# Kernel optimization log

Measured on AMD Instinct MI355X. Metric: run time of the kernel, lower is better.

The kernel has to match this reference:

```python
import jax, jax.numpy as jnp
import numpy as np

T, H, I = 8192, 4096, 11008  # tokens, hidden, intermediate (LLaMA-7B)


def setup_inputs() -> dict:
    key = jax.random.key(0)
    ks = jax.random.split(key, 8)
    # int8-valued tensors stored as int32 (spec dtype enum lacks int8)
    hidden_states = jax.random.randint(ks[0], (T, H), -128, 128, dtype=jnp.int32)
    gate_w = jax.random.randint(ks[1], (I, H), -128, 128, dtype=jnp.int32)
    up_w = jax.random.randint(ks[2], (I, H), -128, 128, dtype=jnp.int32)
    down_w = jax.random.randint(ks[3], (H, I), -128, 128, dtype=jnp.int32)
    # per-tensor dequant scales (alpha = input_scale * weight_scale); small so
    # the SwiGLU product lands roughly in int8 range before requantization
    gate_a = jnp.float32(0.004)
    up_a = jnp.float32(0.004)
    down_a = jnp.float32(0.004)
    gate_b = jax.random.normal(ks[4], (I,), dtype=jnp.float32)
    up_b = jax.random.normal(ks[5], (I,), dtype=jnp.float32)
    down_b = jax.random.normal(ks[6], (H,), dtype=jnp.float32)
    return dict(hidden_states=hidden_states, gate_w=gate_w, gate_a=gate_a,
                gate_b=gate_b, up_w=up_w, up_a=up_a, up_b=up_b,
                down_w=down_w, down_a=down_a, down_b=down_b)


def _w8a8_linear(x_i8, w_i8, alpha, bias):
    # scale alpha and fp32 bias (W8A8BFP32OFP32Linear semantics).
    acc = jnp.matmul(x_i8.astype(jnp.int8), w_i8.astype(jnp.int8).T,
                     preferred_element_type=jnp.int32)
    return acc.astype(jnp.float32) * alpha + bias


def reference(hidden_states, gate_w, gate_a, gate_b, up_w, up_a, up_b,
              down_w, down_a, down_b):
    x1 = jax.nn.silu(_w8a8_linear(hidden_states, gate_w, gate_a, gate_b))  # [T,I]
    x2 = _w8a8_linear(hidden_states, up_w, up_a, up_b)                     # [T,I]
    x = x1 * x2
    # requantize: round, clamp to int8 range
    q = jnp.clip(jnp.round(x), -128.0, 127.0).astype(jnp.int32)
    return _w8a8_linear(q, down_w, down_a, down_b)                          # [T,H]
```

## Files before the change

kernel.cpp:

```cpp
#include <hip/hip_runtime.h>
#include <math.h>

#define T_DIM 8192
#define H_DIM 4096
#define I_DIM 11008

typedef int v4i  __attribute__((ext_vector_type(4)));
typedef int v16i __attribute__((ext_vector_type(16)));

#define AS1(p) ((const __attribute__((address_space(1))) void*)(p))
#define AS3(p) ((__attribute__((address_space(3))) void*)(p))

#define WAIT_VM_BAR(N) asm volatile("s_waitcnt vmcnt(" #N ")\n\ts_barrier" ::: "memory")
#define LGKM0 do { asm volatile("s_waitcnt lgkmcnt(0)" ::: "memory"); \
                   __builtin_amdgcn_sched_barrier(0); } while (0)

__device__ __forceinline__ v4i DSR(const char* p) {
  v4i r;
  unsigned a = (unsigned)(size_t)(const __attribute__((address_space(3))) char*)p;
  asm volatile("ds_read_b128 %0, %1" : "=v"(r) : "v"(a));
  return r;
}

__global__ void pack_i8(const int* __restrict__ src, char* __restrict__ dst, long n16) {
  long i = (long)blockIdx.x * blockDim.x + threadIdx.x;
  long stride = (long)gridDim.x * blockDim.x;
  for (; i < n16; i += stride) {
    const int4* s = (const int4*)src + i * 4;
    int4 a = s[0], b = s[1], c = s[2], d = s[3];
    int w0 = (a.x & 255) | ((a.y & 255) << 8) | ((a.z & 255) << 16) | (a.w << 24);
    int w1 = (b.x & 255) | ((b.y & 255) << 8) | ((b.z & 255) << 16) | (b.w << 24);
    int w2 = (c.x & 255) | ((c.y & 255) << 8) | ((c.z & 255) << 16) | (c.w << 24);
    int w3 = (d.x & 255) | ((d.y & 255) << 8) | ((d.z & 255) << 16) | (d.w << 24);
    ((int4*)dst)[i] = make_int4(w0, w1, w2, w3);
  }
}

#define STG(buf, src, k0, coff) \
  __builtin_amdgcn_global_load_lds(AS1((src) + (k0)), AS3((buf) + (coff) + dd), 16, 0, 0)

__global__ __launch_bounds__(512, 2) void gemm_gateup(
    const char* __restrict__ A, const char* __restrict__ Bg, const char* __restrict__ Bu,
    const float* __restrict__ ga_p, const float* __restrict__ gb,
    const float* __restrict__ ua_p, const float* __restrict__ ub,
    char* __restrict__ Q)
{
  __shared__ char lds[2][65536];
  const int tid = threadIdx.x;
  const int l = tid & 63;
  const int w = tid >> 6;
  const int wm = w >> 2, wn = w & 3;

  const int q8 = 2752 / 8;
  int bid = blockIdx.x;
  int wgid = (bid & 7) * q8 + (bid >> 3);
  int st = wgid >> 3, r = wgid & 7;
  int sm = st / 43, sn = st - sm * 43;
  const int m0 = (sm * 4 + (r & 3)) * 256;
  const int n0 = (sn * 2 + (r >> 2)) * 128;

  v16i accg[4], accu[4];
#pragma unroll
  for (int i = 0; i < 4; ++i) {
#pragma unroll
    for (int j = 0; j < 16; ++j) { accg[i][j] = 0; accu[i][j] = 0; }
  }

  const int r8 = tid >> 3;
  const int gc = ((tid & 7) << 4) ^ ((r8 & 7) << 4);
  const char* pA0 = A  + (size_t)(m0 +       r8) * H_DIM + gc;
  const char* pA1 = A  + (size_t)(m0 +  64 + r8) * H_DIM + gc;
  const char* pA2 = A  + (size_t)(m0 + 128 + r8) * H_DIM + gc;
  const char* pA3 = A  + (size_t)(m0 + 192 + r8) * H_DIM + gc;
  const char* pG0 = Bg + (size_t)(n0 +       r8) * H_DIM + gc;
  const char* pG1 = Bg + (size_t)(n0 +  64 + r8) * H_DIM + gc;
  const char* pU0 = Bu + (size_t)(n0 +       r8) * H_DIM + gc;
  const char* pU1 = Bu + (size_t)(n0 +  64 + r8) * H_DIM + gc;
  const int dd = tid * 16;

  const int li32 = l & 31, kg2 = l >> 5;
  int oA[4][4], oB[4];
#pragma unroll
  for (int ks = 0; ks < 4; ++ks) {
    int slot = (((ks * 2 + kg2) ^ (li32 & 7)) << 4);
#pragma unroll
    for (int mi = 0; mi < 4; ++mi) oA[ks][mi] = (wm * 128 + mi * 32 + li32) * 128 + slot;
    oB[ks] = (wn * 32 + li32) * 128 + slot;
  }

  const int nk = H_DIM / 128;

  {
    char* B0 = lds[0];
    STG(B0, pA0, 0, 0);     STG(B0, pA1, 0, 8192);  STG(B0, pA2, 0, 16384); STG(B0, pA3, 0, 24576);
    STG(B0, pG0, 0, 32768); STG(B0, pG1, 0, 40960); STG(B0, pU0, 0, 49152); STG(B0, pU1, 0, 57344);
    WAIT_VM_BAR(0);
  }

#define GUPH(ks, ...)                                                                    \
  do {                                                                                   \
    v4i gf = DSR(L + 32768 + oB[ks]);                                                    \
    v4i uf = DSR(L + 49152 + oB[ks]);                                                    \
    v4i a0 = DSR(L + oA[ks][0]);                                                         \
    v4i a1 = DSR(L + oA[ks][1]);                                                         \
    v4i a2 = DSR(L + oA[ks][2]);                                                         \
    v4i a3 = DSR(L + oA[ks][3]);                                                         \
    __VA_ARGS__                                                                          \
    LGKM0;                                                                               \
    __builtin_amdgcn_s_setprio(1);                                                       \
    accg[0] = __builtin_amdgcn_mfma_i32_32x32x32_i8(a0, gf, accg[0], 0, 0, 0);           \
    accu[0] = __builtin_amdgcn_mfma_i32_32x32x32_i8(a0, uf, accu[0], 0, 0, 0);           \
    accg[1] = __builtin_amdgcn_mfma_i32_32x32x32_i8(a1, gf, accg[1], 0, 0, 0);           \
    accu[1] = __builtin_amdgcn_mfma_i32_32x32x32_i8(a1, uf, accu[1], 0, 0, 0);           \
    accg[2] = __builtin_amdgcn_mfma_i32_32x32x32_i8(a2, gf, accg[2], 0, 0, 0);           \
    accu[2] = __builtin_amdgcn_mfma_i32_32x32x32_i8(a2, uf, accu[2], 0, 0, 0);           \
    accg[3] = __builtin_amdgcn_mfma_i32_32x32x32_i8(a3, gf, accg[3], 0, 0, 0);           \
    accu[3] = __builtin_amdgcn_mfma_i32_32x32x32_i8(a3, uf, accu[3], 0, 0, 0);           \
    __builtin_amdgcn_s_setprio(0);                                                       \
  } while (0)

  for (int t = 0; t < nk; ++t) {
    const char* L = lds[t & 1];
    char* SB = lds[(t & 1) ^ 1];
    const bool son = (t + 1) < nk;
    const int sk = (t + 1) * 128;

    GUPH(0, if (son) { STG(SB, pA0, sk, 0);     STG(SB, pA1, sk, 8192);
                       STG(SB, pA2, sk, 16384); STG(SB, pA3, sk, 24576); });
    GUPH(1, if (son) { STG(SB, pG0, sk, 32768); STG(SB, pG1, sk, 40960);
                       STG(SB, pU0, sk, 49152); STG(SB, pU1, sk, 57344); });
    GUPH(2, );
    GUPH(3, );
    WAIT_VM_BAR(0);
  }
#undef GUPH

  const float ga = *ga_p, ua = *ua_p;
  const int col = n0 + wn * 32 + li32;
  const float gbv = gb[col], ubv = ub[col];
#pragma unroll
  for (int mi = 0; mi < 4; ++mi) {
    const int rowb = m0 + wm * 128 + mi * 32 + kg2 * 4;
#pragma unroll
    for (int rq = 0; rq < 4; ++rq) {
#pragma unroll
      for (int rr = 0; rr < 4; ++rr) {
        const int rg = rq * 4 + rr;
        float g = (float)accg[mi][rg] * ga + gbv;
        float u = (float)accu[mi][rg] * ua + ubv;
        float x1 = g / (1.0f + expf(-g));
        float x = rintf(x1 * u);
        x = fminf(fmaxf(x, -128.0f), 127.0f);
        Q[(size_t)(rowb + rq * 8 + rr) * I_DIM + col] = (char)(int)x;
      }
    }
  }
}

__global__ __launch_bounds__(512, 2) void gemm_down(
    const char* __restrict__ Qm, const char* __restrict__ Bd,
    const float* __restrict__ da_p, const float* __restrict__ db,
    float* __restrict__ out)
{
  __shared__ char lds[2][65536];
  const int tid = threadIdx.x;
  const int l = tid & 63;
  const int w = tid >> 6;
  const int wm = w >> 2, wn = w & 3;

  const int q8 = 512 / 8;
  int bid = blockIdx.x;
  int wgid = (bid & 7) * q8 + (bid >> 3);
  int st = wgid >> 3, r = wgid & 7;
  int sm = st >> 3, sn = st & 7;
  const int m0 = (sm * 4 + (r & 3)) * 256;
  const int n0 = (sn * 2 + (r >> 2)) * 256;

  v16i acc[4][2];
#pragma unroll
  for (int i = 0; i < 4; ++i) {
#pragma unroll
    for (int n = 0; n < 2; ++n) {
#pragma unroll
      for (int j = 0; j < 16; ++j) acc[i][n][j] = 0;
    }
  }

  const int r8 = tid >> 3;
  const int gc = ((tid & 7) << 4) ^ ((r8 & 7) << 4);
  const char* pA0 = Qm + (size_t)(m0 +       r8) * I_DIM + gc;
  const char* pA1 = Qm + (size_t)(m0 +  64 + r8) * I_DIM + gc;
  const char* pA2 = Qm + (size_t)(m0 + 128 + r8) * I_DIM + gc;
  const char* pA3 = Qm + (size_t)(m0 + 192 + r8) * I_DIM + gc;
  const char* pB0 = Bd + (size_t)(n0 +       r8) * I_DIM + gc;
  const char* pB1 = Bd + (size_t)(n0 +  64 + r8) * I_DIM + gc;
  const char* pB2 = Bd + (size_t)(n0 + 128 + r8) * I_DIM + gc;
  const char* pB3 = Bd + (size_t)(n0 + 192 + r8) * I_DIM + gc;
  const int dd = tid * 16;

  const int li32 = l & 31, kg2 = l >> 5;
  int oA[4][4], oB[4][2];
#pragma unroll
  for (int ks = 0; ks < 4; ++ks) {
    int slot = (((ks * 2 + kg2) ^ (li32 & 7)) << 4);
#pragma unroll
    for (int mi = 0; mi < 4; ++mi) oA[ks][mi] = (wm * 128 + mi * 32 + li32) * 128 + slot;
#pragma unroll
    for (int ni = 0; ni < 2; ++ni) oB[ks][ni] = (wn * 64 + ni * 32 + li32) * 128 + slot;
  }

  const int nk = I_DIM / 128;

  {
    char* B0 = lds[0];
    STG(B0, pA0, 0, 0);     STG(B0, pA1, 0, 8192);  STG(B0, pA2, 0, 16384); STG(B0, pA3, 0, 24576);
    STG(B0, pB0, 0, 32768); STG(B0, pB1, 0, 40960); STG(B0, pB2, 0, 49152); STG(B0, pB3, 0, 57344);
    WAIT_VM_BAR(0);
  }

#define DNPH(ks, ...)                                                                    \
  do {                                                                                   \
    v4i bf0 = DSR(L + 32768 + oB[ks][0]);                                                \
    v4i bf1 = DSR(L + 32768 + oB[ks][1]);                                                \
    v4i a0 = DSR(L + oA[ks][0]);                                                         \
    v4i a1 = DSR(L + oA[ks][1]);                                                         \
    v4i a2 = DSR(L + oA[ks][2]);                                                         \
    v4i a3 = DSR(L + oA[ks][3]);                                                         \
    __VA_ARGS__                                                                          \
    LGKM0;                                                                               \
    __builtin_amdgcn_s_setprio(1);                                                       \
    acc[0][0] = __builtin_amdgcn_mfma_i32_32x32x32_i8(a0, bf0, acc[0][0], 0, 0, 0);      \
    acc[0][1] = __builtin_amdgcn_mfma_i32_32x32x32_i8(a0, bf1, acc[0][1], 0, 0, 0);      \
    acc[1][0] = __builtin_amdgcn_mfma_i32_32x32x32_i8(a1, bf0, acc[1][0], 0, 0, 0);      \
    acc[1][1] = __builtin_amdgcn_mfma_i32_32x32x32_i8(a1, bf1, acc[1][1], 0, 0, 0);      \
    acc[2][0] = __builtin_amdgcn_mfma_i32_32x32x32_i8(a2, bf0, acc[2][0], 0, 0, 0);      \
    acc[2][1] = __builtin_amdgcn_mfma_i32_32x32x32_i8(a2, bf1, acc[2][1], 0, 0, 0);      \
    acc[3][0] = __builtin_amdgcn_mfma_i32_32x32x32_i8(a3, bf0, acc[3][0], 0, 0, 0);      \
    acc[3][1] = __builtin_amdgcn_mfma_i32_32x32x32_i8(a3, bf1, acc[3][1], 0, 0, 0);      \
    __builtin_amdgcn_s_setprio(0);                                                       \
  } while (0)

  for (int t = 0; t < nk; ++t) {
    const char* L = lds[t & 1];
    char* SB = lds[(t & 1) ^ 1];
    const bool son = (t + 1) < nk;
    const int sk = (t + 1) * 128;

    DNPH(0, if (son) { STG(SB, pA0, sk, 0);     STG(SB, pA1, sk, 8192);
                       STG(SB, pA2, sk, 16384); STG(SB, pA3, sk, 24576); });
    DNPH(1, if (son) { STG(SB, pB0, sk, 32768); STG(SB, pB1, sk, 40960);
                       STG(SB, pB2, sk, 49152); STG(SB, pB3, sk, 57344); });
    DNPH(2, );
    DNPH(3, );
    WAIT_VM_BAR(0);
  }
#undef DNPH

  const float da = *da_p;
#pragma unroll
  for (int ni = 0; ni < 2; ++ni) {
    const int col = n0 + wn * 64 + ni * 32 + li32;
    const float dbv = db[col];
#pragma unroll
    for (int mi = 0; mi < 4; ++mi) {
      const int rowb = m0 + wm * 128 + mi * 32 + kg2 * 4;
#pragma unroll
      for (int rq = 0; rq < 4; ++rq) {
#pragma unroll
        for (int rr = 0; rr < 4; ++rr)
          out[(size_t)(rowb + rq * 8 + rr) * H_DIM + col] =
              (float)acc[mi][ni][rq * 4 + rr] * da + dbv;
      }
    }
  }
}

extern "C" void kernel_launch(void* const* d_in, const int* in_sizes, int n_in,
                              void* d_out, int out_size, void* d_ws, size_t ws_size,
                              hipStream_t stream) {
  const int*   hs = (const int*)d_in[0];
  const int*   gw = (const int*)d_in[1];
  const float* ga = (const float*)d_in[2];
  const float* gb = (const float*)d_in[3];
  const int*   uw = (const int*)d_in[4];
  const float* ua = (const float*)d_in[5];
  const float* ub = (const float*)d_in[6];
  const int*   dw = (const int*)d_in[7];
  const float* da = (const float*)d_in[8];
  const float* db = (const float*)d_in[9];

  char* ws   = (char*)d_ws;
  char* hid8 = ws;
  char* g8   = hid8 + (size_t)T_DIM * H_DIM;
  char* u8   = g8   + (size_t)I_DIM * H_DIM;
  char* d8   = u8   + (size_t)I_DIM * H_DIM;
  char* q8   = d8   + (size_t)I_DIM * H_DIM;

  pack_i8<<<2048, 256, 0, stream>>>(hs, hid8, (long)T_DIM * H_DIM / 16);
  pack_i8<<<2048, 256, 0, stream>>>(gw, g8,   (long)I_DIM * H_DIM / 16);
  pack_i8<<<2048, 256, 0, stream>>>(uw, u8,   (long)I_DIM * H_DIM / 16);
  pack_i8<<<2048, 256, 0, stream>>>(dw, d8,   (long)I_DIM * H_DIM / 16);

  gemm_gateup<<<2752, 512, 0, stream>>>(hid8, g8, u8, ga, gb, ua, ub, q8);
  gemm_down<<<512, 512, 0, stream>>>(q8, d8, da, db, (float*)d_out);
}
```

Baseline: 1.164 ms.

## Pre-shuffle int8 operands into MFMA fragment layout and load directly to registers

```diff
diff --git a/kernel.cpp b/kernel.cpp
--- a/kernel.cpp
+++ b/kernel.cpp
@@ -8,36 +8,37 @@
 typedef int v4i  __attribute__((ext_vector_type(4)));
 typedef int v16i __attribute__((ext_vector_type(16)));
 
-#define AS1(p) ((const __attribute__((address_space(1))) void*)(p))
-#define AS3(p) ((__attribute__((address_space(3))) void*)(p))
-
-#define WAIT_VM_BAR(N) asm volatile("s_waitcnt vmcnt(" #N ")\n\ts_barrier" ::: "memory")
-#define LGKM0 do { asm volatile("s_waitcnt lgkmcnt(0)" ::: "memory"); \
-                   __builtin_amdgcn_sched_barrier(0); } while (0)
-
-__device__ __forceinline__ v4i DSR(const char* p) {
-  v4i r;
-  unsigned a = (unsigned)(size_t)(const __attribute__((address_space(3))) char*)p;
-  asm volatile("ds_read_b128 %0, %1" : "=v"(r) : "v"(a));
-  return r;
-}
-
-__global__ void pack_i8(const int* __restrict__ src, char* __restrict__ dst, long n16) {
-  long i = (long)blockIdx.x * blockDim.x + threadIdx.x;
+#define MFMA8 __builtin_amdgcn_mfma_i32_32x32x32_i8
+
+__device__ __forceinline__ v4i LD(const char* base, unsigned off) {
+  return *(const v4i*)(base + off);
+}
+
+__device__ __forceinline__ const char* rflp(const void* p) {
+  unsigned lo = __builtin_amdgcn_readfirstlane((unsigned)(unsigned long long)p);
+  unsigned hi = __builtin_amdgcn_readfirstlane((unsigned)((unsigned long long)p >> 32));
+  return (const char*)(((unsigned long long)hi << 32) | lo);
+}
+
+__global__ void pack_shuf(const int* __restrict__ src, char* __restrict__ dst,
+                          int nk32, long nchunk) {
+  long c = (long)blockIdx.x * blockDim.x + threadIdx.x;
   long stride = (long)gridDim.x * blockDim.x;
-  for (; i < n16; i += stride) {
-    const int4* s = (const int4*)src + i * 4;
-    int4 a = s[0], b = s[1], c = s[2], d = s[3];
+  for (; c < nchunk; c += stride) {
+    int lane = (int)(c & 63);
+    long rk = c >> 6;
+    long r32 = rk / nk32;
+    int k32 = (int)(rk - r32 * nk32);
+    const int4* s = (const int4*)(src + (r32 * 32 + (lane & 31)) * (long)(nk32 * 32)
+                                      + (long)k32 * 32 + ((lane >> 5) << 4));
+    int4 a = s[0], b = s[1], cc = s[2], d = s[3];
     int w0 = (a.x & 255) | ((a.y & 255) << 8) | ((a.z & 255) << 16) | (a.w << 24);
     int w1 = (b.x & 255) | ((b.y & 255) << 8) | ((b.z & 255) << 16) | (b.w << 24);
-    int w2 = (c.x & 255) | ((c.y & 255) << 8) | ((c.z & 255) << 16) | (c.w << 24);
+    int w2 = (cc.x & 255) | ((cc.y & 255) << 8) | ((cc.z & 255) << 16) | (cc.w << 24);
     int w3 = (d.x & 255) | ((d.y & 255) << 8) | ((d.z & 255) << 16) | (d.w << 24);
-    ((int4*)dst)[i] = make_int4(w0, w1, w2, w3);
-  }
-}
-
-#define STG(buf, src, k0, coff) \
-  __builtin_amdgcn_global_load_lds(AS1((src) + (k0)), AS3((buf) + (coff) + dd), 16, 0, 0)
+    ((int4*)dst)[c] = make_int4(w0, w1, w2, w3);
+  }
+}
 
 __global__ __launch_bounds__(512, 2) void gemm_gateup(
     const char* __restrict__ A, const char* __restrict__ Bg, const char* __restrict__ Bu,
@@ -45,11 +46,11 @@
     const float* __restrict__ ua_p, const float* __restrict__ ub,
     char* __restrict__ Q)
 {
-  __shared__ char lds[2][65536];
   const int tid = threadIdx.x;
   const int l = tid & 63;
   const int w = tid >> 6;
   const int wm = w >> 2, wn = w & 3;
+  const int li32 = l & 31, kg2 = l >> 5;
 
   const int q8 = 2752 / 8;
   int bid = blockIdx.x;
@@ -59,6 +60,8 @@
   const int m0 = (sm * 4 + (r & 3)) * 256;
   const int n0 = (sn * 2 + (r >> 2)) * 128;
 
+  const int NK = H_DIM / 32;
+
   v16i accg[4], accu[4];
 #pragma unroll
   for (int i = 0; i < 4; ++i) {
@@ -66,92 +69,80 @@
     for (int j = 0; j < 16; ++j) { accg[i][j] = 0; accu[i][j] = 0; }
   }
 
-  const int r8 = tid >> 3;
-  const int gc = ((tid & 7) << 4) ^ ((r8 & 7) << 4);
-  const char* pA0 = A  + (size_t)(m0 +       r8) * H_DIM + gc;
-  const char* pA1 = A  + (size_t)(m0 +  64 + r8) * H_DIM + gc;
-  const char* pA2 = A  + (size_t)(m0 + 128 + r8) * H_DIM + gc;
-  const char* pA3 = A  + (size_t)(m0 + 192 + r8) * H_DIM + gc;
-  const char* pG0 = Bg + (size_t)(n0 +       r8) * H_DIM + gc;
-  const char* pG1 = Bg + (size_t)(n0 +  64 + r8) * H_DIM + gc;
-  const char* pU0 = Bu + (size_t)(n0 +       r8) * H_DIM + gc;
-  const char* pU1 = Bu + (size_t)(n0 +  64 + r8) * H_DIM + gc;
-  const int dd = tid * 16;
-
-  const int li32 = l & 31, kg2 = l >> 5;
-  int oA[4][4], oB[4];
-#pragma unroll
-  for (int ks = 0; ks < 4; ++ks) {
-    int slot = (((ks * 2 + kg2) ^ (li32 & 7)) << 4);
-#pragma unroll
-    for (int mi = 0; mi < 4; ++mi) oA[ks][mi] = (wm * 128 + mi * 32 + li32) * 128 + slot;
-    oB[ks] = (wn * 32 + li32) * 128 + slot;
-  }
-
-  const int nk = H_DIM / 128;
-
-  {
-    char* B0 = lds[0];
-    STG(B0, pA0, 0, 0);     STG(B0, pA1, 0, 8192);  STG(B0, pA2, 0, 16384); STG(B0, pA3, 0, 24576);
-    STG(B0, pG0, 0, 32768); STG(B0, pG1, 0, 40960); STG(B0, pU0, 0, 49152); STG(B0, pU1, 0, 57344);
-    WAIT_VM_BAR(0);
-  }
-
-#define GUPH(ks, ...)                                                                    \
-  do {                                                                                   \
-    v4i gf = DSR(L + 32768 + oB[ks]);                                                    \
-    v4i uf = DSR(L + 49152 + oB[ks]);                                                    \
-    v4i a0 = DSR(L + oA[ks][0]);                                                         \
-    v4i a1 = DSR(L + oA[ks][1]);                                                         \
-    v4i a2 = DSR(L + oA[ks][2]);                                                         \
-    v4i a3 = DSR(L + oA[ks][3]);                                                         \
-    __VA_ARGS__                                                                          \
-    LGKM0;                                                                               \
-    __builtin_amdgcn_s_setprio(1);                                                       \
-    accg[0] = __builtin_amdgcn_mfma_i32_32x32x32_i8(a0, gf, accg[0], 0, 0, 0);           \
-    accu[0] = __builtin_amdgcn_mfma_i32_32x32x32_i8(a0, uf, accu[0], 0, 0, 0);           \
-    accg[1] = __builtin_amdgcn_mfma_i32_32x32x32_i8(a1, gf, accg[1], 0, 0, 0);           \
-    accu[1] = __builtin_amdgcn_mfma_i32_32x32x32_i8(a1, uf, accu[1], 0, 0, 0);           \
-    accg[2] = __builtin_amdgcn_mfma_i32_32x32x32_i8(a2, gf, accg[2], 0, 0, 0);           \
-    accu[2] = __builtin_amdgcn_mfma_i32_32x32x32_i8(a2, uf, accu[2], 0, 0, 0);           \
-    accg[3] = __builtin_amdgcn_mfma_i32_32x32x32_i8(a3, gf, accg[3], 0, 0, 0);           \
-    accu[3] = __builtin_amdgcn_mfma_i32_32x32x32_i8(a3, uf, accu[3], 0, 0, 0);           \
-    __builtin_amdgcn_s_setprio(0);                                                       \
-  } while (0)
-
-  for (int t = 0; t < nk; ++t) {
-    const char* L = lds[t & 1];
-    char* SB = lds[(t & 1) ^ 1];
-    const bool son = (t + 1) < nk;
-    const int sk = (t + 1) * 128;
-
-    GUPH(0, if (son) { STG(SB, pA0, sk, 0);     STG(SB, pA1, sk, 8192);
-                       STG(SB, pA2, sk, 16384); STG(SB, pA3, sk, 24576); });
-    GUPH(1, if (son) { STG(SB, pG0, sk, 32768); STG(SB, pG1, sk, 40960);
-                       STG(SB, pU0, sk, 49152); STG(SB, pU1, sk, 57344); });
-    GUPH(2, );
-    GUPH(3, );
-    WAIT_VM_BAR(0);
-  }
-#undef GUPH
+  const int r32b = (m0 >> 5) + wm * 4;
+  const char* bA0 = rflp(A + ((size_t)(r32b + 0) * NK << 10));
+  const char* bA1 = rflp(A + ((size_t)(r32b + 1) * NK << 10));
+  const char* bA2 = rflp(A + ((size_t)(r32b + 2) * NK << 10));
+  const char* bA3 = rflp(A + ((size_t)(r32b + 3) * NK << 10));
+  const int n32 = (n0 >> 5) + wn;
+  const char* bG = rflp(Bg + ((size_t)n32 * NK << 10));
+  const char* bU = rflp(Bu + ((size_t)n32 * NK << 10));
+
+  unsigned vp = (unsigned)(l * 16);
+  const unsigned vmax = (unsigned)((NK - 1) * 1024 + l * 16);
+
+  v4i X0, X1, X2, X3, Xg, Xu;
+  v4i Y0, Y1, Y2, Y3, Yg, Yu;
+  v4i Z0, Z1, Z2, Z3, Zg, Zu;
+
+#define ISSUE_GU(S)                                                       \
+  do {                                                                    \
+    unsigned vo = vp < vmax ? vp : vmax;                                  \
+    S##0 = LD(bA0, vo); S##1 = LD(bA1, vo);                               \
+    S##2 = LD(bA2, vo); S##3 = LD(bA3, vo);                               \
+    S##g = LD(bG, vo);  S##u = LD(bU, vo);                                \
+    vp += 1024;                                                           \
+  } while (0)
+
+#define MM_GU(S)                                                          \
+  do {                                                                    \
+    __builtin_amdgcn_s_setprio(1);                                        \
+    accg[0] = MFMA8(S##0, S##g, accg[0], 0, 0, 0);                        \
+    accu[0] = MFMA8(S##0, S##u, accu[0], 0, 0, 0);                        \
+    accg[1] = MFMA8(S##1, S##g, accg[1], 0, 0, 0);                        \
+    accu[1] = MFMA8(S##1, S##u, accu[1], 0, 0, 0);                        \
+    accg[2] = MFMA8(S##2, S##g, accg[2], 0, 0, 0);                        \
+    accu[2] = MFMA8(S##2, S##u, accu[2], 0, 0, 0);                        \
+    accg[3] = MFMA8(S##3, S##g, accg[3], 0, 0, 0);                        \
+    accu[3] = MFMA8(S##3, S##u, accu[3], 0, 0, 0);                        \
+    __builtin_amdgcn_s_setprio(0);                                        \
+  } while (0)
+
+  ISSUE_GU(X); ISSUE_GU(Y); ISSUE_GU(Z);
+
+  for (int it = 0; it < 42; ++it) {
+    MM_GU(X); ISSUE_GU(X);
+    MM_GU(Y); ISSUE_GU(Y);
+    MM_GU(Z); ISSUE_GU(Z);
+  }
+  MM_GU(X);
+  MM_GU(Y);
+#undef ISSUE_GU
+#undef MM_GU
 
   const float ga = *ga_p, ua = *ua_p;
   const int col = n0 + wn * 32 + li32;
   const float gbv = gb[col], ubv = ub[col];
+  const int k32q = (n0 >> 5) + wn;
+  const int lanehi = ((li32 >> 4) & 1) << 5;
+  const int bytelo = li32 & 15;
+  const int NKQ = I_DIM / 32;
 #pragma unroll
   for (int mi = 0; mi < 4; ++mi) {
-    const int rowb = m0 + wm * 128 + mi * 32 + kg2 * 4;
+    const int r32q = (m0 >> 5) + wm * 4 + mi;
+    char* qbase = Q + ((size_t)(r32q * NKQ + k32q) << 10);
 #pragma unroll
     for (int rq = 0; rq < 4; ++rq) {
 #pragma unroll
       for (int rr = 0; rr < 4; ++rr) {
         const int rg = rq * 4 + rr;
+        const int rowin = kg2 * 4 + rq * 8 + rr;
         float g = (float)accg[mi][rg] * ga + gbv;
         float u = (float)accu[mi][rg] * ua + ubv;
         float x1 = g / (1.0f + expf(-g));
         float x = rintf(x1 * u);
         x = fminf(fmaxf(x, -128.0f), 127.0f);
-        Q[(size_t)(rowb + rq * 8 + rr) * I_DIM + col] = (char)(int)x;
+        qbase[((rowin | lanehi) << 4) + bytelo] = (char)(int)x;
       }
     }
   }
@@ -162,11 +153,11 @@
     const float* __restrict__ da_p, const float* __restrict__ db,
     float* __restrict__ out)
 {
-  __shared__ char lds[2][65536];
   const int tid = threadIdx.x;
   const int l = tid & 63;
   const int w = tid >> 6;
   const int wm = w >> 2, wn = w & 3;
+  const int li32 = l & 31, kg2 = l >> 5;
 
   const int q8 = 512 / 8;
   int bid = blockIdx.x;
@@ -176,6 +167,8 @@
   const int m0 = (sm * 4 + (r & 3)) * 256;
   const int n0 = (sn * 2 + (r >> 2)) * 256;
 
+  const int NK = I_DIM / 32;
+
   v16i acc[4][2];
 #pragma unroll
   for (int i = 0; i < 4; ++i) {
@@ -186,75 +179,56 @@
     }
   }
 
-  const int r8 = tid >> 3;
-  const int gc = ((tid & 7) << 4) ^ ((r8 & 7) << 4);
-  const char* pA0 = Qm + (size_t)(m0 +       r8) * I_DIM + gc;
-  const char* pA1 = Qm + (size_t)(m0 +  64 + r8) * I_DIM + gc;
-  const char* pA2 = Qm + (size_t)(m0 + 128 + r8) * I_DIM + gc;
-  const char* pA3 = Qm + (size_t)(m0 + 192 + r8) * I_DIM + gc;
-  const char* pB0 = Bd + (size_t)(n0 +       r8) * I_DIM + gc;
-  const char* pB1 = Bd + (size_t)(n0 +  64 + r8) * I_DIM + gc;
-  const char* pB2 = Bd + (size_t)(n0 + 128 + r8) * I_DIM + gc;
-  const char* pB3 = Bd + (size_t)(n0 + 192 + r8) * I_DIM + gc;
-  const int dd = tid * 16;
-
-  const int li32 = l & 31, kg2 = l >> 5;
-  int oA[4][4], oB[4][2];
-#pragma unroll
-  for (int ks = 0; ks < 4; ++ks) {
-    int slot = (((ks * 2 + kg2) ^ (li32 & 7)) << 4);
-#pragma unroll
-    for (int mi = 0; mi < 4; ++mi) oA[ks][mi] = (wm * 128 + mi * 32 + li32) * 128 + slot;
-#pragma unroll
-    for (int ni = 0; ni < 2; ++ni) oB[ks][ni] = (wn * 64 + ni * 32 + li32) * 128 + slot;
-  }
-
-  const int nk = I_DIM / 128;
-
-  {
-    char* B0 = lds[0];
-    STG(B0, pA0, 0, 0);     STG(B0, pA1, 0, 8192);  STG(B0, pA2, 0, 16384); STG(B0, pA3, 0, 24576);
-    STG(B0, pB0, 0, 32768); STG(B0, pB1, 0, 40960); STG(B0, pB2, 0, 49152); STG(B0, pB3, 0, 57344);
-    WAIT_VM_BAR(0);
-  }
-
-#define DNPH(ks, ...)                                                                    \
-  do {                                                                                   \
-    v4i bf0 = DSR(L + 32768 + oB[ks][0]);                                                \
-    v4i bf1 = DSR(L + 32768 + oB[ks][1]);                                                \
-    v4i a0 = DSR(L + oA[ks][0]);                                                         \
-    v4i a1 = DSR(L + oA[ks][1]);                                                         \
-    v4i a2 = DSR(L + oA[ks][2]);                                                         \
-    v4i a3 = DSR(L + oA[ks][3]);                                                         \
-    __VA_ARGS__                                                                          \
-    LGKM0;                                                                               \
-    __builtin_amdgcn_s_setprio(1);                                                       \
-    acc[0][0] = __builtin_amdgcn_mfma_i32_32x32x32_i8(a0, bf0, acc[0][0], 0, 0, 0);      \
-    acc[0][1] = __builtin_amdgcn_mfma_i32_32x32x32_i8(a0, bf1, acc[0][1], 0, 0, 0);      \
-    acc[1][0] = __builtin_amdgcn_mfma_i32_32x32x32_i8(a1, bf0, acc[1][0], 0, 0, 0);      \
-    acc[1][1] = __builtin_amdgcn_mfma_i32_32x32x32_i8(a1, bf1, acc[1][1], 0, 0, 0);      \
-    acc[2][0] = __builtin_amdgcn_mfma_i32_32x32x32_i8(a2, bf0, acc[2][0], 0, 0, 0);      \
-    acc[2][1] = __builtin_amdgcn_mfma_i32_32x32x32_i8(a2, bf1, acc[2][1], 0, 0, 0);      \
-    acc[3][0] = __builtin_amdgcn_mfma_i32_32x32x32_i8(a3, bf0, acc[3][0], 0, 0, 0);      \
-    acc[3][1] = __builtin_amdgcn_mfma_i32_32x32x32_i8(a3, bf1, acc[3][1], 0, 0, 0);      \
-    __builtin_amdgcn_s_setprio(0);                                                       \
-  } while (0)
-
-  for (int t = 0; t < nk; ++t) {
-    const char* L = lds[t & 1];
-    char* SB = lds[(t & 1) ^ 1];
-    const bool son = (t + 1) < nk;
-    const int sk = (t + 1) * 128;
-
-    DNPH(0, if (son) { STG(SB, pA0, sk, 0);     STG(SB, pA1, sk, 8192);
-                       STG(SB, pA2, sk, 16384); STG(SB, pA3, sk, 24576); });
-    DNPH(1, if (son) { STG(SB, pB0, sk, 32768); STG(SB, pB1, sk, 40960);
-                       STG(SB, pB2, sk, 49152); STG(SB, pB3, sk, 57344); });
-    DNPH(2, );
-    DNPH(3, );
-    WAIT_VM_BAR(0);
-  }
-#undef DNPH
+  const int r32b = (m0 >> 5) + wm * 4;
+  const char* bA0 = rflp(Qm + ((size_t)(r32b + 0) * NK << 10));
+  const char* bA1 = rflp(Qm + ((size_t)(r32b + 1) * NK << 10));
+  const char* bA2 = rflp(Qm + ((size_t)(r32b + 2) * NK << 10));
+  const char* bA3 = rflp(Qm + ((size_t)(r32b + 3) * NK << 10));
+  const int n32b = (n0 >> 5) + wn * 2;
+  const char* bB0 = rflp(Bd + ((size_t)(n32b + 0) * NK << 10));
+  const char* bB1 = rflp(Bd + ((size_t)(n32b + 1) * NK << 10));
+
+  unsigned vp = (unsigned)(l * 16);
+  const unsigned vmax = (unsigned)((NK - 1) * 1024 + l * 16);
+
+  v4i X0, X1, X2, X3, Xb0, Xb1;
+  v4i Y0, Y1, Y2, Y3, Yb0, Yb1;
+  v4i Z0, Z1, Z2, Z3, Zb0, Zb1;
+
+#define ISSUE_DN(S)                                                       \
+  do {                                                                    \
+    unsigned vo = vp < vmax ? vp : vmax;                                  \
+    S##0 = LD(bA0, vo);  S##1 = LD(bA1, vo);                              \
+    S##2 = LD(bA2, vo);  S##3 = LD(bA3, vo);                              \
+    S##b0 = LD(bB0, vo); S##b1 = LD(bB1, vo);                             \
+    vp += 1024;                                                           \
+  } while (0)
+
+#define MM_DN(S)                                                          \
+  do {                                                                    \
+    __builtin_amdgcn_s_setprio(1);                                        \
+    acc[0][0] = MFMA8(S##0, S##b0, acc[0][0], 0, 0, 0);                   \
+    acc[0][1] = MFMA8(S##0, S##b1, acc[0][1], 0, 0, 0);                   \
+    acc[1][0] = MFMA8(S##1, S##b0, acc[1][0], 0, 0, 0);                   \
+    acc[1][1] = MFMA8(S##1, S##b1, acc[1][1], 0, 0, 0);                   \
+    acc[2][0] = MFMA8(S##2, S##b0, acc[2][0], 0, 0, 0);                   \
+    acc[2][1] = MFMA8(S##2, S##b1, acc[2][1], 0, 0, 0);                   \
+    acc[3][0] = MFMA8(S##3, S##b0, acc[3][0], 0, 0, 0);                   \
+    acc[3][1] = MFMA8(S##3, S##b1, acc[3][1], 0, 0, 0);                   \
+    __builtin_amdgcn_s_setprio(0);                                        \
+  } while (0)
+
+  ISSUE_DN(X); ISSUE_DN(Y); ISSUE_DN(Z);
+
+  for (int it = 0; it < 114; ++it) {
+    MM_DN(X); ISSUE_DN(X);
+    MM_DN(Y); ISSUE_DN(Y);
+    MM_DN(Z); ISSUE_DN(Z);
+  }
+  MM_DN(X);
+  MM_DN(Y);
+#undef ISSUE_DN
+#undef MM_DN
 
   const float da = *da_p;
 #pragma unroll
@@ -290,17 +264,17 @@
   const float* db = (const float*)d_in[9];
 
   char* ws   = (char*)d_ws;
-  char* hid8 = ws;
-  char* g8   = hid8 + (size_t)T_DIM * H_DIM;
-  char* u8   = g8   + (size_t)I_DIM * H_DIM;
-  char* d8   = u8   + (size_t)I_DIM * H_DIM;
-  char* q8   = d8   + (size_t)I_DIM * H_DIM;
-
-  pack_i8<<<2048, 256, 0, stream>>>(hs, hid8, (long)T_DIM * H_DIM / 16);
-  pack_i8<<<2048, 256, 0, stream>>>(gw, g8,   (long)I_DIM * H_DIM / 16);
-  pack_i8<<<2048, 256, 0, stream>>>(uw, u8,   (long)I_DIM * H_DIM / 16);
-  pack_i8<<<2048, 256, 0, stream>>>(dw, d8,   (long)I_DIM * H_DIM / 16);
-
-  gemm_gateup<<<2752, 512, 0, stream>>>(hid8, g8, u8, ga, gb, ua, ub, q8);
-  gemm_down<<<512, 512, 0, stream>>>(q8, d8, da, db, (float*)d_out);
-}
+  char* hidS = ws;
+  char* gS   = hidS + (size_t)T_DIM * H_DIM;
+  char* uS   = gS   + (size_t)I_DIM * H_DIM;
+  char* dS   = uS   + (size_t)I_DIM * H_DIM;
+  char* qS   = dS   + (size_t)H_DIM * I_DIM;
+
+  pack_shuf<<<2048, 256, 0, stream>>>(hs, hidS, H_DIM / 32, (long)T_DIM * H_DIM / 16);
+  pack_shuf<<<2048, 256, 0, stream>>>(gw, gS,   H_DIM / 32, (long)I_DIM * H_DIM / 16);
+  pack_shuf<<<2048, 256, 0, stream>>>(uw, uS,   H_DIM / 32, (long)I_DIM * H_DIM / 16);
+  pack_shuf<<<2048, 256, 0, stream>>>(dw, dS,   I_DIM / 32, (long)H_DIM * I_DIM / 16);
+
+  gemm_gateup<<<2752, 512, 0, stream>>>(hidS, gS, uS, ga, gb, ua, ub, qS);
+  gemm_down<<<512, 512, 0, stream>>>(qS, dS, da, db, (float*)d_out);
+}
```

New measurement: 1.384 ms. 18.9% more time.
